# Kernel tuning notes

Hardware: AMD Instinct MI355X
Metric: run time of the kernel (lower is better)

Reference implementation:

```python
import jax, jax.numpy as jnp
import numpy as np

B, S, E, H = 4, 1024, 1024, 16
HD = E // H

def setup_inputs() -> dict:
    key = jax.random.key(0)
    ks = jax.random.split(key, 12)
    std = 1.0 / np.sqrt(E)
    inp = {
        "query": jax.random.normal(ks[0], (B, S, E), jnp.float32),
        "key_t": jax.random.normal(ks[1], (B, S, E), jnp.float32),
        "value": jax.random.normal(ks[2], (B, S, E), jnp.float32),
        # causal mask, broadcastable to (B, H, S, S); 0 => masked
        "mask": jnp.tril(jnp.ones((S, S), jnp.int32))[None, None],
        "Wq": jax.random.normal(ks[3], (E, E), jnp.float32) * std,
        "bq": jnp.zeros((E,), jnp.float32),
        "Wk": jax.random.normal(ks[4], (E, E), jnp.float32) * std,
        "bk": jnp.zeros((E,), jnp.float32),
        "Wv": jax.random.normal(ks[5], (E, E), jnp.float32) * std,
        "bv": jnp.zeros((E,), jnp.float32),
        "Wo": jax.random.normal(ks[6], (E, E), jnp.float32) * std,
        "bo": jnp.zeros((E,), jnp.float32),
    }
    return inp

def reference(query, key_t, value, mask, Wq, bq, Wk, bk, Wv, bv, Wo, bo):
    scale = jnp.asarray(np.sqrt(HD), query.dtype)
    # projections (torch Linear: x @ W.T + b), split into heads -> (B, H, S, HD)
    def split_heads(x):
        return x.reshape(B, S, H, HD).transpose(0, 2, 1, 3)
    q = split_heads(query @ Wq.T + bq)
    k = split_heads(key_t @ Wk.T + bk)
    v = split_heads(value @ Wv.T + bv)
    scores = jnp.einsum("bhqd,bhkd->bhqk", q, k) / scale  # (B,H,S,S)
    scores = jnp.where(mask == 0, jnp.asarray(-jnp.inf, scores.dtype), scores)
    attn = jax.nn.softmax(scores, axis=-1)
    # dropout is identity in eval / p=0
    out = jnp.einsum("bhqk,bhkd->bhqd", attn, v)
    out = out.transpose(0, 2, 1, 3).reshape(B, S, E)
    out = out @ Wo.T + bo
    return out, attn
```

## Files before the change

### kernel.cpp

```cpp
#include <hip/hip_runtime.h>
#include <hip/hip_bf16.h>


typedef short bf16x8 __attribute__((ext_vector_type(8)));
typedef float f32x4 __attribute__((ext_vector_type(4)));

__device__ __forceinline__ unsigned short f2bf(float f) {
  union { float f; unsigned u; } v; v.f = f;
  unsigned r = v.u + 0x7FFF + ((v.u >> 16) & 1);
  return (unsigned short)(r >> 16);
}

__device__ __forceinline__ void gload16(const unsigned short* g, unsigned short* l) {
  __builtin_amdgcn_global_load_lds(
      (const __attribute__((address_space(1))) unsigned int*)g,
      (__attribute__((address_space(3))) unsigned int*)l, 16, 0, 0);
}

__global__ __launch_bounds__(256) void cast3_k(
    const float* __restrict__ a, const float* __restrict__ b,
    const float* __restrict__ c,
    unsigned short* __restrict__ oa, unsigned short* __restrict__ ob,
    unsigned short* __restrict__ oc) {
  const float* in = blockIdx.y == 0 ? a : blockIdx.y == 1 ? b : c;
  unsigned short* out = blockIdx.y == 0 ? oa : blockIdx.y == 1 ? ob : oc;
  int i = (blockIdx.x * 256 + threadIdx.x) * 8;
  float4 x = *(const float4*)(in + i);
  float4 y = *(const float4*)(in + i + 4);
  unsigned short t[8] = { f2bf(x.x), f2bf(x.y), f2bf(x.z), f2bf(x.w),
                          f2bf(y.x), f2bf(y.y), f2bf(y.z), f2bf(y.w) };
  *(bf16x8*)(out + i) = *(bf16x8*)t;
}

__global__ __launch_bounds__(256) void cast4_k(
    const float* __restrict__ a, const float* __restrict__ b,
    const float* __restrict__ c, const float* __restrict__ d,
    unsigned short* __restrict__ oa, unsigned short* __restrict__ ob,
    unsigned short* __restrict__ oc, unsigned short* __restrict__ od) {
  const float* in = blockIdx.y == 0 ? a : blockIdx.y == 1 ? b : blockIdx.y == 2 ? c : d;
  unsigned short* out = blockIdx.y == 0 ? oa : blockIdx.y == 1 ? ob : blockIdx.y == 2 ? oc : od;
  int i = (blockIdx.x * 256 + threadIdx.x) * 8;
  float4 x = *(const float4*)(in + i);
  float4 y = *(const float4*)(in + i + 4);
  unsigned short t[8] = { f2bf(x.x), f2bf(x.y), f2bf(x.z), f2bf(x.w),
                          f2bf(y.x), f2bf(y.y), f2bf(y.z), f2bf(y.w) };
  *(bf16x8*)(out + i) = *(bf16x8*)t;
}

__device__ __forceinline__ void gemm_core(
    const unsigned short* __restrict__ A, const unsigned short* __restrict__ W,
    int m0, int n0, int K, unsigned short* As, unsigned short* Bs, f32x4 acc[4][4])
{
  const int tid = threadIdx.x;
  const int w = tid >> 6, lane = tid & 63, quad = lane >> 4, lc = lane & 15;
  const int wm = (w >> 1) * 64, wn = (w & 1) * 64;
  const int lrow = lane >> 3, lg = lane & 7;

  for (int kb = 0; kb < K; kb += 64) {
#pragma unroll
    for (int t = 0; t < 4; t++) {
      int row = w * 32 + t * 8 + lrow;
      int gsw = lg ^ (row & 7);
      gload16(&A[(size_t)(m0 + row) * K + kb + gsw * 8], &As[(w * 32 + t * 8) * 64]);
      gload16(&W[(size_t)(n0 + row) * K + kb + gsw * 8], &Bs[(w * 32 + t * 8) * 64]);
    }
    __syncthreads();
#pragma unroll
    for (int kk = 0; kk < 2; kk++) {
      bf16x8 af[4], bfr[4];
#pragma unroll
      for (int i = 0; i < 4; i++) {
        int ra = wm + i * 16 + lc;
        af[i] = *(const bf16x8*)&As[ra * 64 + (((kk * 4 + quad) ^ (ra & 7)) * 8)];
      }
#pragma unroll
      for (int j = 0; j < 4; j++) {
        int rb = wn + j * 16 + lc;
        bfr[j] = *(const bf16x8*)&Bs[rb * 64 + (((kk * 4 + quad) ^ (rb & 7)) * 8)];
      }
#pragma unroll
      for (int i = 0; i < 4; i++)
#pragma unroll
        for (int j = 0; j < 4; j++)
          acc[i][j] = __builtin_amdgcn_mfma_f32_16x16x32_bf16(af[i], bfr[j], acc[i][j], 0, 0, 0);
    }
    __syncthreads();
  }
}

__global__ __launch_bounds__(256) void gemm_qkv(
    const unsigned short* __restrict__ Xq, const unsigned short* __restrict__ Xk,
    const unsigned short* __restrict__ Xv,
    const unsigned short* __restrict__ Wq, const unsigned short* __restrict__ Wk,
    const unsigned short* __restrict__ Wv,
    const float* __restrict__ bq, const float* __restrict__ bk, const float* __restrict__ bv,
    unsigned short* __restrict__ Qb, unsigned short* __restrict__ Kb,
    unsigned short* __restrict__ Vt)
{
  __shared__ __align__(16) unsigned short As[128 * 64];
  __shared__ __align__(16) unsigned short Bs[128 * 64];
  const int z = blockIdx.z;
  const unsigned short* A = z == 0 ? Xq : z == 1 ? Xk : Xv;
  const unsigned short* W = z == 0 ? Wq : z == 1 ? Wk : Wv;
  const float* bias = z == 0 ? bq : z == 1 ? bk : bv;
  unsigned short* outRM = z == 0 ? Qb : Kb;
  const int m0 = blockIdx.x * 128, n0 = blockIdx.y * 128;
  const int tid = threadIdx.x;
  const int w = tid >> 6, lane = tid & 63, quad = lane >> 4, lc = lane & 15;
  const int wm = (w >> 1) * 64, wn = (w & 1) * 64;

  f32x4 acc[4][4] = {};
  gemm_core(A, W, m0, n0, 1024, As, Bs, acc);

#pragma unroll
  for (int j = 0; j < 4; j++) {
    int col = n0 + wn + j * 16 + lc;
    float bvl = bias[col];
#pragma unroll
    for (int i = 0; i < 4; i++)
#pragma unroll
      for (int r = 0; r < 4; r++) {
        int row = m0 + wm + i * 16 + quad * 4 + r;
        float v = acc[i][j][r] + bvl;
        if (z < 2)
          outRM[(size_t)row * 1024 + col] = f2bf(v);
        else
          Vt[(((size_t)((row >> 10) * 16 + (col >> 6))) * 64 + (col & 63)) * 1024 + (row & 1023)] = f2bf(v);
      }
  }
}

__global__ __launch_bounds__(256) void gemm_out(
    const unsigned short* __restrict__ A, const unsigned short* __restrict__ W,
    const float* __restrict__ bias, float* __restrict__ outf)
{
  __shared__ __align__(16) unsigned short As[128 * 64];
  __shared__ __align__(16) unsigned short Bs[128 * 64];
  const int m0 = blockIdx.x * 128, n0 = blockIdx.y * 128;
  const int tid = threadIdx.x;
  const int w = tid >> 6, lane = tid & 63, quad = lane >> 4, lc = lane & 15;
  const int wm = (w >> 1) * 64, wn = (w & 1) * 64;

  f32x4 acc[4][4] = {};
  gemm_core(A, W, m0, n0, 1024, As, Bs, acc);

#pragma unroll
  for (int j = 0; j < 4; j++) {
    int col = n0 + wn + j * 16 + lc;
    float bvl = bias[col];
#pragma unroll
    for (int i = 0; i < 4; i++)
#pragma unroll
      for (int r = 0; r < 4; r++) {
        int row = m0 + wm + i * 16 + quad * 4 + r;
        outf[(size_t)row * 1024 + col] = acc[i][j][r] + bvl;
      }
  }
}

__global__ __launch_bounds__(256) void attn_fused(
    const unsigned short* __restrict__ Qb,
    const unsigned short* __restrict__ Kb,
    const unsigned short* __restrict__ Vt,
    float* __restrict__ attn,
    unsigned short* __restrict__ O)
{
  __shared__ __align__(16) unsigned short Pl[4][16][40];
  const int bh = blockIdx.x, b = bh >> 4, h = bh & 15;
  const int q0 = blockIdx.y * 64;
  const int tid = threadIdx.x;
  const int w = tid >> 6, lane = tid & 63, quad = lane >> 4, lc = lane & 15;
  const int g0 = q0 + w * 16;
  const int kt_d = g0 >> 4;

  const unsigned short* qp = Qb + ((size_t)(b * 1024 + g0 + lc)) * 1024 + h * 64 + quad * 8;
  bf16x8 a0 = *(const bf16x8*)qp;
  bf16x8 a1 = *(const bf16x8*)(qp + 32);

  float m_[4] = { -1e30f, -1e30f, -1e30f, -1e30f };
  float l_[4] = { 0.f, 0.f, 0.f, 0.f };

  for (int kt = 0; kt <= kt_d; kt++) {
    int kv0 = kt * 16;
    const unsigned short* kp = Kb + ((size_t)(b * 1024 + kv0 + lc)) * 1024 + h * 64 + quad * 8;
    bf16x8 b0 = *(const bf16x8*)kp;
    bf16x8 b1 = *(const bf16x8*)(kp + 32);
    f32x4 c = {};
    c = __builtin_amdgcn_mfma_f32_16x16x32_bf16(a0, b0, c, 0, 0, 0);
    c = __builtin_amdgcn_mfma_f32_16x16x32_bf16(a1, b1, c, 0, 0, 0);
#pragma unroll
    for (int r = 0; r < 4; r++) {
      int qr = g0 + quad * 4 + r;
      float s = c[r] * 0.125f;
      float sv = (kv0 + lc) > qr ? -1e30f : s;
      float mn = fmaxf(m_[r], sv);
      l_[r] = l_[r] * __expf(m_[r] - mn) + __expf(sv - mn);
      m_[r] = mn;
    }
  }
  float mofs[4];
#pragma unroll
  for (int r = 0; r < 4; r++) {
    float mT = m_[r];
#pragma unroll
    for (int off = 1; off < 16; off <<= 1) mT = fmaxf(mT, __shfl_xor(mT, off));
    float lt = l_[r] * __expf(m_[r] - mT);
#pragma unroll
    for (int off = 1; off < 16; off <<= 1) lt += __shfl_xor(lt, off);
    mofs[r] = mT + __logf(lt);
  }

  float* arow = attn + (size_t)bh * 1024 * 1024;
  f32x4 oacc[4] = {};
  for (int kt2 = 0; kt2 <= kt_d; kt2 += 2) {
#pragma unroll
    for (int tt = 0; tt < 2; tt++) {
      int kt = kt2 + tt;
      int kv0 = kt * 16;
      if (kt <= kt_d) {
        const unsigned short* kp = Kb + ((size_t)(b * 1024 + kv0 + lc)) * 1024 + h * 64 + quad * 8;
        bf16x8 b0 = *(const bf16x8*)kp;
        bf16x8 b1 = *(const bf16x8*)(kp + 32);
        f32x4 c = {};
        c = __builtin_amdgcn_mfma_f32_16x16x32_bf16(a0, b0, c, 0, 0, 0);
        c = __builtin_amdgcn_mfma_f32_16x16x32_bf16(a1, b1, c, 0, 0, 0);
#pragma unroll
        for (int r = 0; r < 4; r++) {
          int qr = g0 + quad * 4 + r;
          float p = (kv0 + lc) > qr ? 0.f : __expf(c[r] * 0.125f - mofs[r]);
          arow[(size_t)qr * 1024 + kv0 + lc] = p;
          Pl[w][quad * 4 + r][tt * 16 + lc] = f2bf(p);
        }
      } else {
#pragma unroll
        for (int r = 0; r < 4; r++) Pl[w][quad * 4 + r][tt * 16 + lc] = 0;
      }
    }
    bf16x8 pa = *(const bf16x8*)&Pl[w][lc][quad * 8];
#pragma unroll
    for (int j = 0; j < 4; j++) {
      const unsigned short* vp = Vt + ((size_t)bh * 64 + j * 16 + lc) * 1024 + kt2 * 16 + quad * 8;
      bf16x8 bv = *(const bf16x8*)vp;
      oacc[j] = __builtin_amdgcn_mfma_f32_16x16x32_bf16(pa, bv, oacc[j], 0, 0, 0);
    }
  }

  {
    int rr = lane >> 2, cl = lane & 3;
    float4 z = make_float4(0.f, 0.f, 0.f, 0.f);
    for (int c0 = g0 + 16 + cl * 4; c0 < 1024; c0 += 16)
      *(float4*)&arow[(size_t)(g0 + rr) * 1024 + c0] = z;
  }

#pragma unroll
  for (int j = 0; j < 4; j++) {
    int d = h * 64 + j * 16 + lc;
#pragma unroll
    for (int r = 0; r < 4; r++) {
      int q = g0 + quad * 4 + r;
      O[((size_t)(b * 1024 + q)) * 1024 + d] = f2bf(oacc[j][r]);
    }
  }
}

extern "C" void kernel_launch(void* const* d_in, const int* in_sizes, int n_in,
                              void* d_out, int out_size, void* d_ws, size_t ws_size,
                              hipStream_t stream) {
  const float* query = (const float*)d_in[0];
  const float* key_t = (const float*)d_in[1];
  const float* value = (const float*)d_in[2];
  const float* Wq = (const float*)d_in[4];
  const float* bq = (const float*)d_in[5];
  const float* Wk = (const float*)d_in[6];
  const float* bk = (const float*)d_in[7];
  const float* Wv = (const float*)d_in[8];
  const float* bv = (const float*)d_in[9];
  const float* Wo = (const float*)d_in[10];
  const float* bo = (const float*)d_in[11];

  unsigned short* Xq  = (unsigned short*)d_ws;
  unsigned short* Xk  = Xq  + 4194304;
  unsigned short* Xv  = Xk  + 4194304;
  unsigned short* Wqb = Xv  + 4194304;
  unsigned short* Wkb = Wqb + 1048576;
  unsigned short* Wvb = Wkb + 1048576;
  unsigned short* Wob = Wvb + 1048576;
  unsigned short* Qb  = Wob + 1048576;
  unsigned short* Kb  = Qb  + 4194304;
  unsigned short* Vtb = Kb  + 4194304;
  unsigned short* Ob  = Vtb + 4194304;

  float* outO = (float*)d_out;
  float* attn = outO + 4194304;

  cast3_k<<<dim3(2048, 3), 256, 0, stream>>>(query, key_t, value, Xq, Xk, Xv);
  cast4_k<<<dim3(512, 4), 256, 0, stream>>>(Wq, Wk, Wv, Wo, Wqb, Wkb, Wvb, Wob);

  gemm_qkv<<<dim3(32, 8, 3), 256, 0, stream>>>(Xq, Xk, Xv, Wqb, Wkb, Wvb,
                                               bq, bk, bv, Qb, Kb, Vtb);

  attn_fused<<<dim3(64, 16), 256, 0, stream>>>(Qb, Kb, Vtb, attn, Ob);

  gemm_out<<<dim3(32, 8), 256, 0, stream>>>(Ob, Wob, bo, outO);
}
```

Before: 548.1 us.

## Stage K/V tiles in LDS, vectorize attn/O/Vt stores, reverse block order

The attention kernel now loads 64-row K and V chunks into swizzled shared memory with async global-to-LDS loads, so the four waves of a block share them instead of each wave fetching K and V straight from global memory. The probability tile is staged in LDS and written to the attention matrix as float4 rows, and O is written as 16-byte vectors through LDS. Mask checks are skipped on tiles that lie fully below the diagonal. Blocks run in reverse query order so the longest causal rows start first, and the V projection writes its transposed output through a swizzled LDS tile with vector stores. The cost is added block-wide barriers and more shared memory per block, which may lower occupancy.

```diff
diff --git a/kernel.cpp b/kernel.cpp
--- a/kernel.cpp
+++ b/kernel.cpp
@@ -97,8 +97,9 @@
     unsigned short* __restrict__ Qb, unsigned short* __restrict__ Kb,
     unsigned short* __restrict__ Vt)
 {
-  __shared__ __align__(16) unsigned short As[128 * 64];
-  __shared__ __align__(16) unsigned short Bs[128 * 64];
+  __shared__ __align__(16) unsigned short S[128 * 136];
+  unsigned short* As = S;
+  unsigned short* Bs = S + 128 * 64;
   const int z = blockIdx.z;
   const unsigned short* A = z == 0 ? Xq : z == 1 ? Xk : Xv;
   const unsigned short* W = z == 0 ? Wq : z == 1 ? Wk : Wv;
@@ -112,21 +113,44 @@
   f32x4 acc[4][4] = {};
   gemm_core(A, W, m0, n0, 1024, As, Bs, acc);
 
-#pragma unroll
-  for (int j = 0; j < 4; j++) {
-    int col = n0 + wn + j * 16 + lc;
-    float bvl = bias[col];
-#pragma unroll
-    for (int i = 0; i < 4; i++)
-#pragma unroll
-      for (int r = 0; r < 4; r++) {
-        int row = m0 + wm + i * 16 + quad * 4 + r;
-        float v = acc[i][j][r] + bvl;
-        if (z < 2)
-          outRM[(size_t)row * 1024 + col] = f2bf(v);
-        else
-          Vt[(((size_t)((row >> 10) * 16 + (col >> 6))) * 64 + (col & 63)) * 1024 + (row & 1023)] = f2bf(v);
-      }
+  if (z < 2) {
+#pragma unroll
+    for (int j = 0; j < 4; j++) {
+      int col = n0 + wn + j * 16 + lc;
+      float bvl = bias[col];
+#pragma unroll
+      for (int i = 0; i < 4; i++)
+#pragma unroll
+        for (int r = 0; r < 4; r++) {
+          int row = m0 + wm + i * 16 + quad * 4 + r;
+          outRM[(size_t)row * 1024 + col] = f2bf(acc[i][j][r] + bvl);
+        }
+    }
+  } else {
+    unsigned short* T = S;
+#pragma unroll
+    for (int j = 0; j < 4; j++) {
+      int col = wn + j * 16 + lc;
+      float bvl = bias[n0 + col];
+#pragma unroll
+      for (int i = 0; i < 4; i++)
+#pragma unroll
+        for (int r = 0; r < 4; r++) {
+          int row = wm + i * 16 + quad * 4 + r;
+          T[col * 136 + (((row >> 3) ^ (col & 7)) << 3) + (row & 7)] =
+              f2bf(acc[i][j][r] + bvl);
+        }
+    }
+    __syncthreads();
+    const int b_ = m0 >> 10, sb = m0 & 1023;
+#pragma unroll
+    for (int it = 0; it < 8; it++) {
+      int cl = w * 32 + it * 4 + (lane >> 4);
+      int sg = lane & 15;
+      int colg = n0 + cl;
+      *(bf16x8*)&Vt[((size_t)((b_ * 16 + (colg >> 6)) * 64 + (colg & 63))) * 1024 + sb + sg * 8] =
+          *(const bf16x8*)&T[cl * 136 + ((sg ^ (cl & 7)) << 3)];
+    }
   }
 }
 
@@ -165,13 +189,19 @@
     float* __restrict__ attn,
     unsigned short* __restrict__ O)
 {
+  __shared__ __align__(16) unsigned short Ks[64 * 64];
+  __shared__ __align__(16) unsigned short Vs[64 * 64];
   __shared__ __align__(16) unsigned short Pl[4][16][40];
+  __shared__ __align__(16) float          Ps[4][16][36];
   const int bh = blockIdx.x, b = bh >> 4, h = bh & 15;
-  const int q0 = blockIdx.y * 64;
+  const int by = (int)gridDim.y - 1 - (int)blockIdx.y;
+  const int q0 = by * 64;
   const int tid = threadIdx.x;
   const int w = tid >> 6, lane = tid & 63, quad = lane >> 4, lc = lane & 15;
   const int g0 = q0 + w * 16;
   const int kt_d = g0 >> 4;
+  const int nch = by + 1;
+  const int sr = lane >> 3, sg = lane & 7;
 
   const unsigned short* qp = Qb + ((size_t)(b * 1024 + g0 + lc)) * 1024 + h * 64 + quad * 8;
   bf16x8 a0 = *(const bf16x8*)qp;
@@ -180,24 +210,48 @@
   float m_[4] = { -1e30f, -1e30f, -1e30f, -1e30f };
   float l_[4] = { 0.f, 0.f, 0.f, 0.f };
 
-  for (int kt = 0; kt <= kt_d; kt++) {
-    int kv0 = kt * 16;
-    const unsigned short* kp = Kb + ((size_t)(b * 1024 + kv0 + lc)) * 1024 + h * 64 + quad * 8;
-    bf16x8 b0 = *(const bf16x8*)kp;
-    bf16x8 b1 = *(const bf16x8*)(kp + 32);
-    f32x4 c = {};
-    c = __builtin_amdgcn_mfma_f32_16x16x32_bf16(a0, b0, c, 0, 0, 0);
-    c = __builtin_amdgcn_mfma_f32_16x16x32_bf16(a1, b1, c, 0, 0, 0);
-#pragma unroll
-    for (int r = 0; r < 4; r++) {
-      int qr = g0 + quad * 4 + r;
-      float s = c[r] * 0.125f;
-      float sv = (kv0 + lc) > qr ? -1e30f : s;
-      float mn = fmaxf(m_[r], sv);
-      l_[r] = l_[r] * __expf(m_[r] - mn) + __expf(sv - mn);
-      m_[r] = mn;
-    }
-  }
+  for (int c = 0; c < nch; c++) {
+    int kv0 = c * 64;
+    {
+      int r0 = w * 8 + sr, r1 = 32 + r0;
+      gload16(&Kb[((size_t)(b * 1024 + kv0 + r0)) * 1024 + h * 64 + (sg ^ (r0 & 7)) * 8],
+              &Ks[(w * 8) * 64]);
+      gload16(&Kb[((size_t)(b * 1024 + kv0 + r1)) * 1024 + h * 64 + (sg ^ (r1 & 7)) * 8],
+              &Ks[(32 + w * 8) * 64]);
+    }
+    __syncthreads();
+    int tmax = kt_d - c * 4;
+    int tlim = tmax < 3 ? tmax : 3;
+    for (int t = 0; t <= tlim; t++) {
+      int rk = t * 16 + lc;
+      const unsigned short* kr = &Ks[rk * 64];
+      bf16x8 b0 = *(const bf16x8*)&kr[((quad ^ (rk & 7))) * 8];
+      bf16x8 b1 = *(const bf16x8*)&kr[(((quad + 4) ^ (rk & 7))) * 8];
+      f32x4 cc = {};
+      cc = __builtin_amdgcn_mfma_f32_16x16x32_bf16(a0, b0, cc, 0, 0, 0);
+      cc = __builtin_amdgcn_mfma_f32_16x16x32_bf16(a1, b1, cc, 0, 0, 0);
+      if (t < tmax) {
+#pragma unroll
+        for (int r = 0; r < 4; r++) {
+          float s = cc[r] * 0.125f;
+          float mn = fmaxf(m_[r], s);
+          l_[r] = l_[r] * __expf(m_[r] - mn) + __expf(s - mn);
+          m_[r] = mn;
+        }
+      } else {
+#pragma unroll
+        for (int r = 0; r < 4; r++) {
+          int qr = g0 + quad * 4 + r;
+          float sv = (kv0 + t * 16 + lc) > qr ? -1e30f : cc[r] * 0.125f;
+          float mn = fmaxf(m_[r], sv);
+          l_[r] = l_[r] * __expf(m_[r] - mn) + __expf(sv - mn);
+          m_[r] = mn;
+        }
+      }
+    }
+    __syncthreads();
+  }
+
   float mofs[4];
 #pragma unroll
   for (int r = 0; r < 4; r++) {
@@ -212,37 +266,63 @@
 
   float* arow = attn + (size_t)bh * 1024 * 1024;
   f32x4 oacc[4] = {};
-  for (int kt2 = 0; kt2 <= kt_d; kt2 += 2) {
-#pragma unroll
-    for (int tt = 0; tt < 2; tt++) {
-      int kt = kt2 + tt;
-      int kv0 = kt * 16;
-      if (kt <= kt_d) {
-        const unsigned short* kp = Kb + ((size_t)(b * 1024 + kv0 + lc)) * 1024 + h * 64 + quad * 8;
-        bf16x8 b0 = *(const bf16x8*)kp;
-        bf16x8 b1 = *(const bf16x8*)(kp + 32);
-        f32x4 c = {};
-        c = __builtin_amdgcn_mfma_f32_16x16x32_bf16(a0, b0, c, 0, 0, 0);
-        c = __builtin_amdgcn_mfma_f32_16x16x32_bf16(a1, b1, c, 0, 0, 0);
-#pragma unroll
-        for (int r = 0; r < 4; r++) {
-          int qr = g0 + quad * 4 + r;
-          float p = (kv0 + lc) > qr ? 0.f : __expf(c[r] * 0.125f - mofs[r]);
-          arow[(size_t)qr * 1024 + kv0 + lc] = p;
-          Pl[w][quad * 4 + r][tt * 16 + lc] = f2bf(p);
-        }
-      } else {
-#pragma unroll
-        for (int r = 0; r < 4; r++) Pl[w][quad * 4 + r][tt * 16 + lc] = 0;
-      }
-    }
-    bf16x8 pa = *(const bf16x8*)&Pl[w][lc][quad * 8];
-#pragma unroll
-    for (int j = 0; j < 4; j++) {
-      const unsigned short* vp = Vt + ((size_t)bh * 64 + j * 16 + lc) * 1024 + kt2 * 16 + quad * 8;
-      bf16x8 bv = *(const bf16x8*)vp;
-      oacc[j] = __builtin_amdgcn_mfma_f32_16x16x32_bf16(pa, bv, oacc[j], 0, 0, 0);
-    }
+  for (int c = 0; c < nch; c++) {
+    int kv0 = c * 64;
+    {
+      int r0 = w * 8 + sr, r1 = 32 + r0;
+      gload16(&Kb[((size_t)(b * 1024 + kv0 + r0)) * 1024 + h * 64 + (sg ^ (r0 & 7)) * 8],
+              &Ks[(w * 8) * 64]);
+      gload16(&Kb[((size_t)(b * 1024 + kv0 + r1)) * 1024 + h * 64 + (sg ^ (r1 & 7)) * 8],
+              &Ks[(32 + w * 8) * 64]);
+      gload16(&Vt[((size_t)(bh * 64 + r0)) * 1024 + kv0 + (sg ^ (r0 & 7)) * 8],
+              &Vs[(w * 8) * 64]);
+      gload16(&Vt[((size_t)(bh * 64 + r1)) * 1024 + kv0 + (sg ^ (r1 & 7)) * 8],
+              &Vs[(32 + w * 8) * 64]);
+    }
+    __syncthreads();
+    int tmax = kt_d - c * 4;
+#pragma unroll
+    for (int u = 0; u < 2; u++) {
+      if (u * 2 <= tmax) {
+#pragma unroll
+        for (int t2 = 0; t2 < 2; t2++) {
+          int t = u * 2 + t2;
+          if (t <= tmax) {
+            int rk = t * 16 + lc;
+            const unsigned short* kr = &Ks[rk * 64];
+            bf16x8 b0 = *(const bf16x8*)&kr[((quad ^ (rk & 7))) * 8];
+            bf16x8 b1 = *(const bf16x8*)&kr[(((quad + 4) ^ (rk & 7))) * 8];
+            f32x4 cc = {};
+            cc = __builtin_amdgcn_mfma_f32_16x16x32_bf16(a0, b0, cc, 0, 0, 0);
+            cc = __builtin_amdgcn_mfma_f32_16x16x32_bf16(a1, b1, cc, 0, 0, 0);
+#pragma unroll
+            for (int r = 0; r < 4; r++) {
+              int qr = g0 + quad * 4 + r;
+              float p = (kv0 + t * 16 + lc) > qr ? 0.f : __expf(cc[r] * 0.125f - mofs[r]);
+              Ps[w][quad * 4 + r][t2 * 16 + lc] = p;
+              Pl[w][quad * 4 + r][t2 * 16 + lc] = f2bf(p);
+            }
+          } else {
+#pragma unroll
+            for (int r = 0; r < 4; r++) Pl[w][quad * 4 + r][t2 * 16 + lc] = 0;
+          }
+        }
+        bf16x8 pa = *(const bf16x8*)&Pl[w][lc][quad * 8];
+#pragma unroll
+        for (int j = 0; j < 4; j++) {
+          int hd = j * 16 + lc;
+          bf16x8 bv = *(const bf16x8*)&Vs[hd * 64 + (((u * 4 + quad) ^ (hd & 7)) * 8)];
+          oacc[j] = __builtin_amdgcn_mfma_f32_16x16x32_bf16(pa, bv, oacc[j], 0, 0, 0);
+        }
+        int nt = tmax - u * 2 + 1; if (nt > 2) nt = 2;
+        int srow = lane >> 2, cf = (lane & 3) * 4;
+        float* dst = &arow[(size_t)(g0 + srow) * 1024 + kv0 + u * 32];
+        *(float4*)(dst + cf) = *(const float4*)&Ps[w][srow][cf];
+        if (nt == 2)
+          *(float4*)(dst + 16 + cf) = *(const float4*)&Ps[w][srow][16 + cf];
+      }
+    }
+    __syncthreads();
   }
 
   {
@@ -252,13 +332,18 @@
       *(float4*)&arow[(size_t)(g0 + rr) * 1024 + c0] = z;
   }
 
-#pragma unroll
-  for (int j = 0; j < 4; j++) {
-    int d = h * 64 + j * 16 + lc;
-#pragma unroll
-    for (int r = 0; r < 4; r++) {
-      int q = g0 + quad * 4 + r;
-      O[((size_t)(b * 1024 + q)) * 1024 + d] = f2bf(oacc[j][r]);
+  {
+    unsigned short* ob = (unsigned short*)&Ps[w][0][0];
+#pragma unroll
+    for (int j = 0; j < 4; j++)
+#pragma unroll
+      for (int r = 0; r < 4; r++)
+        ob[(quad * 4 + r) * 72 + j * 16 + lc] = f2bf(oacc[j][r]);
+#pragma unroll
+    for (int it = 0; it < 2; it++) {
+      int row = it * 8 + (lane >> 3), off = (lane & 7) * 8;
+      *(bf16x8*)&O[((size_t)(b * 1024 + g0 + row)) * 1024 + h * 64 + off] =
+          *(const bf16x8*)&ob[row * 72 + off];
     }
   }
 }
```

Measured after the change: 482.3 us. 1.14x faster.
